# Kernel optimization log

Measured on AMD Instinct MI355X. Metric: run time of the kernel, lower is better.

Reference implementation:

```python
import jax, jax.numpy as jnp
import numpy as np


def setup_inputs() -> dict:
    key = jax.random.key(0)
    k1, k2 = jax.random.split(key)
    T, D, E = 8192, 4096, 64
    x = jax.random.normal(k1, (T, D), dtype=jnp.float32)
    gate_w = jax.random.normal(k2, (E, D), dtype=jnp.float32) * (1.0 / np.sqrt(D))
    return {"x": x, "gate_w": gate_w}


def reference(x, gate_w):
    TOPK = 8
    # logits = x @ W^T, computed in float32 like .float() in torch
    logits = jnp.einsum('td,ed->te', x, gate_w).astype(jnp.float32)
    scores = jax.nn.sigmoid(scores_in := logits) if False else jax.nn.sigmoid(logits)
    # top-k scores per token; values are exactly the gathered weights
    weights, indices = jax.lax.top_k(scores, TOPK)
    weights = weights / jnp.clip(jnp.sum(weights, axis=-1, keepdims=True), 1e-12)
    return weights.astype(x.dtype), indices
```

## Files before the change

### kernel.cpp

```cpp
#include <hip/hip_runtime.h>
#include <math.h>

#define T_TOTAL 8192
#define D_TOTAL 4096
#define E 64
#define TOPK 8
#define NKB (D_TOTAL / 32)

typedef short short8 __attribute__((ext_vector_type(8)));
typedef float f32x4 __attribute__((ext_vector_type(4)));

__device__ __forceinline__ void split3(const float* v8, short8& h, short8& m, short8& l) {
#pragma unroll
    for (int j = 0; j < 8; ++j) {
        const float f = v8[j];
        const unsigned u = __float_as_uint(f);
        const unsigned hu = u & 0xffff0000u;
        const float r1 = f - __uint_as_float(hu);
        const unsigned mu = __float_as_uint(r1) & 0xffff0000u;
        const float r2 = r1 - __uint_as_float(mu);
        const unsigned lu = __float_as_uint(r2);
        h[j] = (short)(hu >> 16);
        m[j] = (short)(mu >> 16);
        l[j] = (short)(lu >> 16);
    }
}

__global__ __launch_bounds__(256)
void prep_w(const float* __restrict__ w, short8* __restrict__ Bh,
            short8* __restrict__ Bm, short8* __restrict__ Bl) {
    const int t = blockIdx.x * 256 + threadIdx.x;
    const int lane = t & 63;
    const int nt = (t >> 6) & 3;
    const int kb = t >> 8;
    const int e = nt * 16 + (lane & 15);
    const int k = kb * 32 + (lane >> 4) * 8;

    const float* src = w + (size_t)e * D_TOTAL + k;
    float v[8];
    *reinterpret_cast<float4*>(&v[0]) = *reinterpret_cast<const float4*>(src);
    *reinterpret_cast<float4*>(&v[4]) = *reinterpret_cast<const float4*>(src + 4);

    short8 h, m, l;
    split3(v, h, m, l);
    Bh[t] = h; Bm[t] = m; Bl[t] = l;
}

#define LOADX(DST, K) {                                                              \
    const float* ap0 = xb + (K);                                                     \
    *reinterpret_cast<float4*>(&(DST)[0])  = *reinterpret_cast<const float4*>(ap0);  \
    *reinterpret_cast<float4*>(&(DST)[4])  = *reinterpret_cast<const float4*>(ap0 + 4); \
    const float* ap1 = ap0 + 16 * D_TOTAL;                                           \
    *reinterpret_cast<float4*>(&(DST)[8])  = *reinterpret_cast<const float4*>(ap1);  \
    *reinterpret_cast<float4*>(&(DST)[12]) = *reinterpret_cast<const float4*>(ap1 + 4); \
}

__global__ __launch_bounds__(1024, 4)
void fused_router(const float* __restrict__ x,
                  const short8* __restrict__ Bh, const short8* __restrict__ Bm,
                  const short8* __restrict__ Bl,
                  float* __restrict__ out) {
    __shared__ float tiles[8 * 2048];
    __shared__ float fin[2048];

    const int tid = threadIdx.x;
    const int lane = tid & 63;
    const int wv = tid >> 6;
    const int tok0 = blockIdx.x * 32;

    const int row = lane & 15;
    const int kq = lane >> 4;

    const float* xb = x + (size_t)(tok0 + row) * D_TOTAL + kq * 8;

    f32x4 acc[2][4];
#pragma unroll
    for (int m = 0; m < 2; ++m)
#pragma unroll
        for (int n = 0; n < 4; ++n) acc[m][n] = (f32x4){0.f, 0.f, 0.f, 0.f};

    const int kbase = wv * 256;

    float xbuf[2][16];
    LOADX(xbuf[0], kbase);

#pragma unroll
    for (int kb = 0; kb < 8; ++kb) {
        const int k = kbase + kb * 32;
        const int gkb = k >> 5;

        short8 bh[4], bm[4], bl[4];
#pragma unroll
        for (int nt = 0; nt < 4; ++nt) {
            const size_t bi = (size_t)(gkb * 4 + nt) * 64 + lane;
            bh[nt] = Bh[bi];
            bm[nt] = Bm[bi];
            bl[nt] = Bl[bi];
        }

        if (kb < 7) LOADX(xbuf[(kb + 1) & 1], k + 32);

#pragma unroll
        for (int m = 0; m < 2; ++m) {
            short8 ah, am_, al;
            split3(&xbuf[kb & 1][m * 8], ah, am_, al);
#pragma unroll
            for (int nt = 0; nt < 4; ++nt) {
                f32x4 c = acc[m][nt];
                c = __builtin_amdgcn_mfma_f32_16x16x32_bf16(ah,  bh[nt], c, 0, 0, 0);
                c = __builtin_amdgcn_mfma_f32_16x16x32_bf16(ah,  bm[nt], c, 0, 0, 0);
                c = __builtin_amdgcn_mfma_f32_16x16x32_bf16(am_, bh[nt], c, 0, 0, 0);
                c = __builtin_amdgcn_mfma_f32_16x16x32_bf16(am_, bm[nt], c, 0, 0, 0);
                c = __builtin_amdgcn_mfma_f32_16x16x32_bf16(ah,  bl[nt], c, 0, 0, 0);
                c = __builtin_amdgcn_mfma_f32_16x16x32_bf16(al,  bh[nt], c, 0, 0, 0);
                acc[m][nt] = c;
            }
        }
    }

    if (wv >= 8) {
        float* s = &tiles[(size_t)(wv - 8) * 2048 + lane];
#pragma unroll
        for (int m = 0; m < 2; ++m)
#pragma unroll
            for (int nt = 0; nt < 4; ++nt)
#pragma unroll
                for (int r = 0; r < 4; ++r)
                    s[(m * 16 + nt * 4 + r) * 64] = acc[m][nt][r];
    }
    __syncthreads();
    if (wv < 8) {
        float* s = &tiles[(size_t)wv * 2048 + lane];
#pragma unroll
        for (int m = 0; m < 2; ++m)
#pragma unroll
            for (int nt = 0; nt < 4; ++nt)
#pragma unroll
                for (int r = 0; r < 4; ++r) {
                    const int j = (m * 16 + nt * 4 + r) * 64;
                    s[j] = acc[m][nt][r] + s[j];
                }
    }
    __syncthreads();

    {
        float s0 = 0.f, s1 = 0.f;
#pragma unroll
        for (int w2 = 0; w2 < 8; ++w2) {
            s0 += tiles[w2 * 2048 + tid];
            s1 += tiles[w2 * 2048 + 1024 + tid];
        }
        const int j = tid >> 6, ln = tid & 63;
        const int t = (ln >> 4) * 4 + (j & 3);
        const int e = ((j >> 2) & 3) * 16 + (ln & 15);
        fin[t * 64 + e] = s0;
        fin[(t + 16) * 64 + e] = s1;
    }
    __syncthreads();

#pragma unroll
    for (int rep = 0; rep < 2; ++rep) {
        const int t = wv * 2 + rep;
        float v = fin[t * 64 + lane];
        float wj[TOPK];
        int   ij[TOPK];
        float wsum = 0.f;
#pragma unroll
        for (int j = 0; j < TOPK; ++j) {
            float mx = v;
#pragma unroll
            for (int off = 32; off >= 1; off >>= 1)
                mx = fmaxf(mx, __shfl_xor(mx, off));
            const unsigned long long msk = __ballot(v == mx);
            const int widx = (int)__builtin_ctzll(msk);
            wj[j] = 1.f / (1.f + expf(-mx));
            ij[j] = widx;
            wsum += wj[j];
            if (lane == widx) v = -INFINITY;
        }
        const float inv = 1.f / fmaxf(wsum, 1e-12f);
        const int tg = tok0 + t;
        if (lane == 0) {
#pragma unroll
            for (int j = 0; j < TOPK; ++j)
                out[(size_t)tg * TOPK + j] = wj[j] * inv;
#pragma unroll
            for (int j = 0; j < TOPK; ++j)
                out[(size_t)T_TOTAL * TOPK + (size_t)tg * TOPK + j] = (float)ij[j];
        }
    }
}

extern "C" void kernel_launch(void* const* d_in, const int* in_sizes, int n_in,
                              void* d_out, int out_size, void* d_ws, size_t ws_size,
                              hipStream_t stream) {
    const float* x = (const float*)d_in[0];
    const float* w = (const float*)d_in[1];
    float* out = (float*)d_out;

    short8* Bh = (short8*)d_ws;
    short8* Bm = Bh + (size_t)NKB * 4 * 64;
    short8* Bl = Bm + (size_t)NKB * 4 * 64;

    prep_w<<<NKB * 4 * 64 / 256, 256, 0, stream>>>(w, Bh, Bm, Bl);
    fused_router<<<T_TOTAL / 32, 1024, 0, stream>>>(x, Bh, Bm, Bl, out);
}
```

Measured before the change: 51.39 us.

## Halve tokens per block, raise occupancy, and vectorise bf16 split with perm

```diff
diff --git a/kernel.cpp b/kernel.cpp
--- a/kernel.cpp
+++ b/kernel.cpp
@@ -26,6 +26,24 @@
     }
 }
 
+__device__ __forceinline__ void split3v(const float* v, short8& h, short8& m, short8& l) {
+    unsigned* hp = reinterpret_cast<unsigned*>(&h);
+    unsigned* mp = reinterpret_cast<unsigned*>(&m);
+    unsigned* lp = reinterpret_cast<unsigned*>(&l);
+#pragma unroll
+    for (int p = 0; p < 4; ++p) {
+        const float a = v[2 * p], b = v[2 * p + 1];
+        const unsigned hw = __builtin_amdgcn_perm(__float_as_uint(b), __float_as_uint(a), 0x07060302u);
+        const float r0 = a - __uint_as_float(hw << 16);
+        const float r1 = b - __uint_as_float(hw & 0xffff0000u);
+        const unsigned mw = __builtin_amdgcn_perm(__float_as_uint(r1), __float_as_uint(r0), 0x07060302u);
+        const float s0 = r0 - __uint_as_float(mw << 16);
+        const float s1 = r1 - __uint_as_float(mw & 0xffff0000u);
+        const unsigned lw = __builtin_amdgcn_perm(__float_as_uint(s1), __float_as_uint(s0), 0x07060302u);
+        hp[p] = hw; mp[p] = mw; lp[p] = lw;
+    }
+}
+
 __global__ __launch_bounds__(256)
 void prep_w(const float* __restrict__ w, short8* __restrict__ Bh,
             short8* __restrict__ Bm, short8* __restrict__ Bl) {
@@ -46,121 +64,101 @@
     Bh[t] = h; Bm[t] = m; Bl[t] = l;
 }
 
-#define LOADX(DST, K) {                                                              \
-    const float* ap0 = xb + (K);                                                     \
-    *reinterpret_cast<float4*>(&(DST)[0])  = *reinterpret_cast<const float4*>(ap0);  \
-    *reinterpret_cast<float4*>(&(DST)[4])  = *reinterpret_cast<const float4*>(ap0 + 4); \
-    const float* ap1 = ap0 + 16 * D_TOTAL;                                           \
-    *reinterpret_cast<float4*>(&(DST)[8])  = *reinterpret_cast<const float4*>(ap1);  \
-    *reinterpret_cast<float4*>(&(DST)[12]) = *reinterpret_cast<const float4*>(ap1 + 4); \
-}
-
-__global__ __launch_bounds__(1024, 4)
+__global__ __launch_bounds__(1024, 8)
 void fused_router(const float* __restrict__ x,
                   const short8* __restrict__ Bh, const short8* __restrict__ Bm,
                   const short8* __restrict__ Bl,
                   float* __restrict__ out) {
-    __shared__ float tiles[8 * 2048];
-    __shared__ float fin[2048];
+    __shared__ float tiles[8 * 1024];
+    __shared__ float fin[1024];
 
     const int tid = threadIdx.x;
     const int lane = tid & 63;
     const int wv = tid >> 6;
-    const int tok0 = blockIdx.x * 32;
+    const int tok0 = blockIdx.x * 16;
 
     const int row = lane & 15;
     const int kq = lane >> 4;
 
     const float* xb = x + (size_t)(tok0 + row) * D_TOTAL + kq * 8;
 
-    f32x4 acc[2][4];
-#pragma unroll
-    for (int m = 0; m < 2; ++m)
-#pragma unroll
-        for (int n = 0; n < 4; ++n) acc[m][n] = (f32x4){0.f, 0.f, 0.f, 0.f};
+    f32x4 acc[4];
+#pragma unroll
+    for (int n = 0; n < 4; ++n) acc[n] = (f32x4){0.f, 0.f, 0.f, 0.f};
 
     const int kbase = wv * 256;
 
-    float xbuf[2][16];
-    LOADX(xbuf[0], kbase);
+    float xr[8];
+    {
+        const float* ap = xb + kbase;
+        *reinterpret_cast<float4*>(&xr[0]) = *reinterpret_cast<const float4*>(ap);
+        *reinterpret_cast<float4*>(&xr[4]) = *reinterpret_cast<const float4*>(ap + 4);
+    }
 
 #pragma unroll
     for (int kb = 0; kb < 8; ++kb) {
         const int k = kbase + kb * 32;
         const int gkb = k >> 5;
 
-        short8 bh[4], bm[4], bl[4];
+        short8 ah, am_, al;
+        split3v(xr, ah, am_, al);
+        if (kb < 7) {
+            const float* ap = xb + k + 32;
+            *reinterpret_cast<float4*>(&xr[0]) = *reinterpret_cast<const float4*>(ap);
+            *reinterpret_cast<float4*>(&xr[4]) = *reinterpret_cast<const float4*>(ap + 4);
+        }
+
 #pragma unroll
         for (int nt = 0; nt < 4; ++nt) {
             const size_t bi = (size_t)(gkb * 4 + nt) * 64 + lane;
-            bh[nt] = Bh[bi];
-            bm[nt] = Bm[bi];
-            bl[nt] = Bl[bi];
-        }
-
-        if (kb < 7) LOADX(xbuf[(kb + 1) & 1], k + 32);
-
-#pragma unroll
-        for (int m = 0; m < 2; ++m) {
-            short8 ah, am_, al;
-            split3(&xbuf[kb & 1][m * 8], ah, am_, al);
-#pragma unroll
-            for (int nt = 0; nt < 4; ++nt) {
-                f32x4 c = acc[m][nt];
-                c = __builtin_amdgcn_mfma_f32_16x16x32_bf16(ah,  bh[nt], c, 0, 0, 0);
-                c = __builtin_amdgcn_mfma_f32_16x16x32_bf16(ah,  bm[nt], c, 0, 0, 0);
-                c = __builtin_amdgcn_mfma_f32_16x16x32_bf16(am_, bh[nt], c, 0, 0, 0);
-                c = __builtin_amdgcn_mfma_f32_16x16x32_bf16(am_, bm[nt], c, 0, 0, 0);
-                c = __builtin_amdgcn_mfma_f32_16x16x32_bf16(ah,  bl[nt], c, 0, 0, 0);
-                c = __builtin_amdgcn_mfma_f32_16x16x32_bf16(al,  bh[nt], c, 0, 0, 0);
-                acc[m][nt] = c;
-            }
+            const short8 bh = Bh[bi];
+            const short8 bm = Bm[bi];
+            const short8 bl = Bl[bi];
+            f32x4 c = acc[nt];
+            c = __builtin_amdgcn_mfma_f32_16x16x32_bf16(ah,  bh, c, 0, 0, 0);
+            c = __builtin_amdgcn_mfma_f32_16x16x32_bf16(ah,  bm, c, 0, 0, 0);
+            c = __builtin_amdgcn_mfma_f32_16x16x32_bf16(am_, bh, c, 0, 0, 0);
+            c = __builtin_amdgcn_mfma_f32_16x16x32_bf16(am_, bm, c, 0, 0, 0);
+            c = __builtin_amdgcn_mfma_f32_16x16x32_bf16(ah,  bl, c, 0, 0, 0);
+            c = __builtin_amdgcn_mfma_f32_16x16x32_bf16(al,  bh, c, 0, 0, 0);
+            acc[nt] = c;
         }
     }
 
     if (wv >= 8) {
-        float* s = &tiles[(size_t)(wv - 8) * 2048 + lane];
-#pragma unroll
-        for (int m = 0; m < 2; ++m)
-#pragma unroll
-            for (int nt = 0; nt < 4; ++nt)
-#pragma unroll
-                for (int r = 0; r < 4; ++r)
-                    s[(m * 16 + nt * 4 + r) * 64] = acc[m][nt][r];
+        float* s = &tiles[(size_t)(wv - 8) * 1024 + lane];
+#pragma unroll
+        for (int nt = 0; nt < 4; ++nt)
+#pragma unroll
+            for (int r = 0; r < 4; ++r)
+                s[(nt * 4 + r) * 64] = acc[nt][r];
     }
     __syncthreads();
     if (wv < 8) {
-        float* s = &tiles[(size_t)wv * 2048 + lane];
-#pragma unroll
-        for (int m = 0; m < 2; ++m)
-#pragma unroll
-            for (int nt = 0; nt < 4; ++nt)
-#pragma unroll
-                for (int r = 0; r < 4; ++r) {
-                    const int j = (m * 16 + nt * 4 + r) * 64;
-                    s[j] = acc[m][nt][r] + s[j];
-                }
+        float* s = &tiles[(size_t)wv * 1024 + lane];
+#pragma unroll
+        for (int nt = 0; nt < 4; ++nt)
+#pragma unroll
+            for (int r = 0; r < 4; ++r) {
+                const int j = (nt * 4 + r) * 64;
+                s[j] = acc[nt][r] + s[j];
+            }
     }
     __syncthreads();
 
     {
-        float s0 = 0.f, s1 = 0.f;
-#pragma unroll
-        for (int w2 = 0; w2 < 8; ++w2) {
-            s0 += tiles[w2 * 2048 + tid];
-            s1 += tiles[w2 * 2048 + 1024 + tid];
-        }
+        float s0 = 0.f;
+#pragma unroll
+        for (int w2 = 0; w2 < 8; ++w2) s0 += tiles[w2 * 1024 + tid];
         const int j = tid >> 6, ln = tid & 63;
         const int t = (ln >> 4) * 4 + (j & 3);
-        const int e = ((j >> 2) & 3) * 16 + (ln & 15);
+        const int e = (j >> 2) * 16 + (ln & 15);
         fin[t * 64 + e] = s0;
-        fin[(t + 16) * 64 + e] = s1;
     }
     __syncthreads();
 
-#pragma unroll
-    for (int rep = 0; rep < 2; ++rep) {
-        const int t = wv * 2 + rep;
+    {
+        const int t = wv;
         float v = fin[t * 64 + lane];
         float wj[TOPK];
         int   ij[TOPK];
@@ -203,5 +201,5 @@
     short8* Bl = Bm + (size_t)NKB * 4 * 64;
 
     prep_w<<<NKB * 4 * 64 / 256, 256, 0, stream>>>(w, Bh, Bm, Bl);
-    fused_router<<<T_TOTAL / 32, 1024, 0, stream>>>(x, Bh, Bm, Bl, out);
-}
+    fused_router<<<T_TOTAL / 16, 1024, 0, stream>>>(x, Bh, Bm, Bl, out);
+}
```

Measured after the change: 58.74 us. 14.3% more time.

## Halve waves per block, double K chunk per wave, vectorize bf16 split

Applied to the files above, without the earlier changes.

```diff
diff --git a/kernel.cpp b/kernel.cpp
--- a/kernel.cpp
+++ b/kernel.cpp
@@ -6,6 +6,10 @@
 #define E 64
 #define TOPK 8
 #define NKB (D_TOTAL / 32)
+
+#define WVS 8
+#define WKCH (D_TOTAL / WVS)
+#define TOKB 32
 
 typedef short short8 __attribute__((ext_vector_type(8)));
 typedef float f32x4 __attribute__((ext_vector_type(4)));
@@ -26,6 +30,24 @@
     }
 }
 
+__device__ __forceinline__ void split3v(const float* v, short8& h, short8& m, short8& l) {
+    unsigned* hp = reinterpret_cast<unsigned*>(&h);
+    unsigned* mp = reinterpret_cast<unsigned*>(&m);
+    unsigned* lp = reinterpret_cast<unsigned*>(&l);
+#pragma unroll
+    for (int p = 0; p < 4; ++p) {
+        const float a = v[2 * p], b = v[2 * p + 1];
+        const unsigned hw = __builtin_amdgcn_perm(__float_as_uint(b), __float_as_uint(a), 0x07060302u);
+        const float r0 = a - __uint_as_float(hw << 16);
+        const float r1 = b - __uint_as_float(hw & 0xffff0000u);
+        const unsigned mw = __builtin_amdgcn_perm(__float_as_uint(r1), __float_as_uint(r0), 0x07060302u);
+        const float s0 = r0 - __uint_as_float(mw << 16);
+        const float s1 = r1 - __uint_as_float(mw & 0xffff0000u);
+        const unsigned lw = __builtin_amdgcn_perm(__float_as_uint(s1), __float_as_uint(s0), 0x07060302u);
+        hp[p] = hw; mp[p] = mw; lp[p] = lw;
+    }
+}
+
 __global__ __launch_bounds__(256)
 void prep_w(const float* __restrict__ w, short8* __restrict__ Bh,
             short8* __restrict__ Bm, short8* __restrict__ Bl) {
@@ -46,32 +68,22 @@
     Bh[t] = h; Bm[t] = m; Bl[t] = l;
 }
 
-#define LOADX(DST, K) {                                                              \
-    const float* ap0 = xb + (K);                                                     \
-    *reinterpret_cast<float4*>(&(DST)[0])  = *reinterpret_cast<const float4*>(ap0);  \
-    *reinterpret_cast<float4*>(&(DST)[4])  = *reinterpret_cast<const float4*>(ap0 + 4); \
-    const float* ap1 = ap0 + 16 * D_TOTAL;                                           \
-    *reinterpret_cast<float4*>(&(DST)[8])  = *reinterpret_cast<const float4*>(ap1);  \
-    *reinterpret_cast<float4*>(&(DST)[12]) = *reinterpret_cast<const float4*>(ap1 + 4); \
-}
-
-__global__ __launch_bounds__(1024, 4)
+__global__ __launch_bounds__(512, 4)
 void fused_router(const float* __restrict__ x,
                   const short8* __restrict__ Bh, const short8* __restrict__ Bm,
                   const short8* __restrict__ Bl,
                   float* __restrict__ out) {
-    __shared__ float tiles[8 * 2048];
+    __shared__ float tiles[4][2048];
     __shared__ float fin[2048];
 
     const int tid = threadIdx.x;
     const int lane = tid & 63;
     const int wv = tid >> 6;
-    const int tok0 = blockIdx.x * 32;
+    const int tok0 = blockIdx.x * TOKB;
 
     const int row = lane & 15;
     const int kq = lane >> 4;
-
-    const float* xb = x + (size_t)(tok0 + row) * D_TOTAL + kq * 8;
+    const float* xb = x + (size_t)(tok0 + row) * D_TOTAL + wv * WKCH + kq * 8;
 
     f32x4 acc[2][4];
 #pragma unroll
@@ -79,47 +91,57 @@
 #pragma unroll
         for (int n = 0; n < 4; ++n) acc[m][n] = (f32x4){0.f, 0.f, 0.f, 0.f};
 
-    const int kbase = wv * 256;
-
-    float xbuf[2][16];
-    LOADX(xbuf[0], kbase);
-
-#pragma unroll
-    for (int kb = 0; kb < 8; ++kb) {
-        const int k = kbase + kb * 32;
-        const int gkb = k >> 5;
-
-        short8 bh[4], bm[4], bl[4];
+    float xr[2][2][8];
+#pragma unroll
+    for (int m = 0; m < 2; ++m) {
+        const float* ap = xb + (size_t)(m * 16) * D_TOTAL;
+        *reinterpret_cast<float4*>(&xr[0][m][0]) = *reinterpret_cast<const float4*>(ap);
+        *reinterpret_cast<float4*>(&xr[0][m][4]) = *reinterpret_cast<const float4*>(ap + 4);
+    }
+
+#pragma unroll
+    for (int kb = 0; kb < 16; ++kb) {
+        const int gkb = wv * 16 + kb;
+
+        short8 bh[4], bm_[4], bl[4];
 #pragma unroll
         for (int nt = 0; nt < 4; ++nt) {
             const size_t bi = (size_t)(gkb * 4 + nt) * 64 + lane;
-            bh[nt] = Bh[bi];
-            bm[nt] = Bm[bi];
-            bl[nt] = Bl[bi];
-        }
-
-        if (kb < 7) LOADX(xbuf[(kb + 1) & 1], k + 32);
+            bh[nt]  = Bh[bi];
+            bm_[nt] = Bm[bi];
+            bl[nt]  = Bl[bi];
+        }
+
+        if (kb < 15) {
+#pragma unroll
+            for (int m = 0; m < 2; ++m) {
+                const float* ap = xb + (size_t)(m * 16) * D_TOTAL + (kb + 1) * 32;
+                *reinterpret_cast<float4*>(&xr[(kb + 1) & 1][m][0]) = *reinterpret_cast<const float4*>(ap);
+                *reinterpret_cast<float4*>(&xr[(kb + 1) & 1][m][4]) = *reinterpret_cast<const float4*>(ap + 4);
+            }
+        }
 
 #pragma unroll
         for (int m = 0; m < 2; ++m) {
             short8 ah, am_, al;
-            split3(&xbuf[kb & 1][m * 8], ah, am_, al);
-#pragma unroll
-            for (int nt = 0; nt < 4; ++nt) {
-                f32x4 c = acc[m][nt];
-                c = __builtin_amdgcn_mfma_f32_16x16x32_bf16(ah,  bh[nt], c, 0, 0, 0);
-                c = __builtin_amdgcn_mfma_f32_16x16x32_bf16(ah,  bm[nt], c, 0, 0, 0);
-                c = __builtin_amdgcn_mfma_f32_16x16x32_bf16(am_, bh[nt], c, 0, 0, 0);
-                c = __builtin_amdgcn_mfma_f32_16x16x32_bf16(am_, bm[nt], c, 0, 0, 0);
-                c = __builtin_amdgcn_mfma_f32_16x16x32_bf16(ah,  bl[nt], c, 0, 0, 0);
-                c = __builtin_amdgcn_mfma_f32_16x16x32_bf16(al,  bh[nt], c, 0, 0, 0);
-                acc[m][nt] = c;
-            }
-        }
-    }
-
-    if (wv >= 8) {
-        float* s = &tiles[(size_t)(wv - 8) * 2048 + lane];
+            split3v(xr[kb & 1][m], ah, am_, al);
+#pragma unroll
+            for (int nt = 0; nt < 4; ++nt) acc[m][nt] = __builtin_amdgcn_mfma_f32_16x16x32_bf16(ah,  bh[nt],  acc[m][nt], 0, 0, 0);
+#pragma unroll
+            for (int nt = 0; nt < 4; ++nt) acc[m][nt] = __builtin_amdgcn_mfma_f32_16x16x32_bf16(ah,  bm_[nt], acc[m][nt], 0, 0, 0);
+#pragma unroll
+            for (int nt = 0; nt < 4; ++nt) acc[m][nt] = __builtin_amdgcn_mfma_f32_16x16x32_bf16(am_, bh[nt],  acc[m][nt], 0, 0, 0);
+#pragma unroll
+            for (int nt = 0; nt < 4; ++nt) acc[m][nt] = __builtin_amdgcn_mfma_f32_16x16x32_bf16(am_, bm_[nt], acc[m][nt], 0, 0, 0);
+#pragma unroll
+            for (int nt = 0; nt < 4; ++nt) acc[m][nt] = __builtin_amdgcn_mfma_f32_16x16x32_bf16(ah,  bl[nt],  acc[m][nt], 0, 0, 0);
+#pragma unroll
+            for (int nt = 0; nt < 4; ++nt) acc[m][nt] = __builtin_amdgcn_mfma_f32_16x16x32_bf16(al,  bh[nt],  acc[m][nt], 0, 0, 0);
+        }
+    }
+
+    if (wv >= 4) {
+        float* s = &tiles[wv - 4][lane];
 #pragma unroll
         for (int m = 0; m < 2; ++m)
 #pragma unroll
@@ -129,8 +151,8 @@
                     s[(m * 16 + nt * 4 + r) * 64] = acc[m][nt][r];
     }
     __syncthreads();
-    if (wv < 8) {
-        float* s = &tiles[(size_t)wv * 2048 + lane];
+    if (wv < 4) {
+        float* s = &tiles[wv][lane];
 #pragma unroll
         for (int m = 0; m < 2; ++m)
 #pragma unroll
@@ -143,24 +165,21 @@
     }
     __syncthreads();
 
-    {
-        float s0 = 0.f, s1 = 0.f;
-#pragma unroll
-        for (int w2 = 0; w2 < 8; ++w2) {
-            s0 += tiles[w2 * 2048 + tid];
-            s1 += tiles[w2 * 2048 + 1024 + tid];
-        }
-        const int j = tid >> 6, ln = tid & 63;
-        const int t = (ln >> 4) * 4 + (j & 3);
+#pragma unroll
+    for (int p = 0; p < 4; ++p) {
+        const int j4 = tid + p * 512;
+        float s0 = tiles[0][j4] + tiles[1][j4];
+        s0 += tiles[2][j4] + tiles[3][j4];
+        const int j = j4 >> 6, ln = j4 & 63;
+        const int t = (j >> 4) * 16 + (ln >> 4) * 4 + (j & 3);
         const int e = ((j >> 2) & 3) * 16 + (ln & 15);
         fin[t * 64 + e] = s0;
-        fin[(t + 16) * 64 + e] = s1;
     }
     __syncthreads();
 
 #pragma unroll
-    for (int rep = 0; rep < 2; ++rep) {
-        const int t = wv * 2 + rep;
+    for (int rep = 0; rep < 4; ++rep) {
+        const int t = wv * 4 + rep;
         float v = fin[t * 64 + lane];
         float wj[TOPK];
         int   ij[TOPK];
@@ -203,5 +222,5 @@
     short8* Bl = Bm + (size_t)NKB * 4 * 64;
 
     prep_w<<<NKB * 4 * 64 / 256, 256, 0, stream>>>(w, Bh, Bm, Bl);
-    fused_router<<<T_TOTAL / 32, 1024, 0, stream>>>(x, Bh, Bm, Bl, out);
-}
+    fused_router<<<T_TOTAL / TOKB, 512, 0, stream>>>(x, Bh, Bm, Bl, out);
+}
```

After: 53.36 us. 1.04x slower.
